# Optimization experiments

Measured on AMD Instinct MI355X. Metric: run time of the kernel, lower is better.

## Reference

```python
import jax, jax.numpy as jnp
import numpy as np

D = 256            # number of graph nodes (example.size(3))
K1 = D // 2        # topkpool1 k
K2 = D // 4        # topkpool2 k
B = 8


def _lrelu(x):
    return jnp.where(x > 0, x, 0.33 * x)


def _e2e(h, wa, ba, wb, bb):
    # h: [B,C,d,d]; wa,wb: [P,C,d] (squeezed (1,d)/(d,1) conv kernels)
    # cnn1: contract over columns j -> [B,P,d]; cnn2: contract over rows i -> [B,P,d]
    a = jnp.einsum('bcij,pcj->bpi', h, wa) + ba[None, :, None]
    b = jnp.einsum('bcij,pci->bpj', h, wb) + bb[None, :, None]
    # cat([a]*d, 3) + cat([b]*d, 2)  ==  broadcast-add
    return a[:, :, :, None] + b[:, :, None, :]


def _gcn(h, g, W, b):
    # h: [B,N,F_in], g: [B,N,N]; faithful to norm_g: g[i,j] / deg[j] (column-normalized
    # because torch broadcasts the [N] degree vector over the LAST dim)
    gb = (g > 0).astype(h.dtype)
    deg = gb.sum(axis=2)                      # [B,N] row sums
    gn = gb / deg[:, None, :]                 # divide column j by deg[j]
    return jnp.einsum('bij,bjf->bif', gn, h) @ W.T + b


def _pool(h, g, s, k):
    # h: [B,N,F], g: [B,N,N], s: [B,N,1] -> top-k nodes by score (descending)
    vals, idx = jax.lax.top_k(s[:, :, 0], k)              # [B,k]
    hn = jnp.take_along_axis(h, idx[:, :, None], axis=1)  # [B,k,F]
    gn = jnp.take_along_axis(g, idx[:, :, None], axis=1)
    gn = jnp.take_along_axis(gn, idx[:, None, :], axis=2) # [B,k,k]
    return hn, gn, vals[:, :, None]


def _readout(h):
    # h: [B,N,F] (node axis = 1); torch ReadOut on [B,F,N,1] max/mean over dim=2
    return jnp.concatenate([h.max(axis=1), h.mean(axis=1)], axis=1)  # [B,2F]


def _forward(x, w1a, b1a, w1b, b1b, w2a, b2a, w2b, b2b, e2n_w, e2n_b,
             a11_w, a11_b, a12_w, a12_b, g1_w, g1_b,
             a21_w, a21_b, a22_w, a22_b,
             d1_w, d1_b, d2_w, d2_b, d3_w, d3_b):
    h = _lrelu(_e2e(x, w1a, b1a, w1b, b1b))         # [B,128,d,d]
    h = _lrelu(_e2e(h, w2a, b2a, w2b, b2b))         # [B,256,d,d]
    # E2N conv (1,d): [B,8,d,1] -> node features [B,d,8]
    nodes = _lrelu(jnp.einsum('bcij,pcj->bpi', h, e2n_w) + e2n_b[None, :, None])
    nodes = jnp.transpose(nodes, (0, 2, 1))          # [B,d,8]
    g0 = x[:, 0]                                     # [B,d,d]

    w = _lrelu(_gcn(nodes, g0, a11_w, a11_b))        # [B,d,1]
    w = jax.nn.sigmoid(_gcn(w, g0, a12_w, a12_b))
    h1, g1, s1 = _pool(nodes, g0, w, K1)             # [B,K1,8], [B,K1,K1], [B,K1,1]
    out = h1 * s1 + h1
    sum1 = _readout(out)                             # [B,16]

    h2 = _gcn(out, g1, g1_w, g1_b)                   # [B,K1,8] (no activation, as in torch)
    w = _lrelu(_gcn(h2, g1, a21_w, a21_b))
    w = jax.nn.sigmoid(_gcn(w, g1, a22_w, a22_b))
    h3, g2, s2 = _pool(h2, g1, w, K2)                # [B,K2,8]
    out2 = h3 * s2 + h3
    sum2 = _readout(out2)                            # [B,16]

    z = sum1 + sum2                                  # [B,16]
    z = _lrelu(z @ d1_w.T + d1_b)                    # dropout = identity (eval mode)
    z = _lrelu(z @ d2_w.T + d2_b)
    return z @ d3_w.T + d3_b                         # [B,1]


def setup_inputs() -> dict:
    key = jax.random.key(0)
    ks = jax.random.split(key, 16)
    f32 = jnp.float32

    def rn(k, shape, scale):
        return jax.random.normal(k, shape, dtype=f32) * scale

    return {
        'x': jax.random.normal(ks[0], (B, 1, D, D), dtype=f32),
        'w1a': rn(ks[1], (128, 1, D), 0.08),  'b1a': jnp.zeros((128,), f32),
        'w1b': rn(ks[2], (128, 1, D), 0.08),  'b1b': jnp.zeros((128,), f32),
        'w2a': rn(ks[3], (256, 128, D), 0.008), 'b2a': jnp.zeros((256,), f32),
        'w2b': rn(ks[4], (256, 128, D), 0.008), 'b2b': jnp.zeros((256,), f32),
        'e2n_w': rn(ks[5], (8, 256, D), 0.005), 'e2n_b': jnp.zeros((8,), f32),
        'a11_w': rn(ks[6], (1, 8), 0.3),  'a11_b': jnp.zeros((1,), f32),
        'a12_w': rn(ks[7], (1, 1), 0.3),  'a12_b': jnp.zeros((1,), f32),
        'g1_w': rn(ks[8], (8, 8), 0.3),   'g1_b': jnp.zeros((8,), f32),
        'a21_w': rn(ks[9], (1, 8), 0.3),  'a21_b': jnp.zeros((1,), f32),
        'a22_w': rn(ks[10], (1, 1), 0.3), 'a22_b': jnp.zeros((1,), f32),
        'd1_w': rn(ks[11], (128, 16), 0.2), 'd1_b': jnp.zeros((128,), f32),
        'd2_w': rn(ks[12], (64, 128), 0.08), 'd2_b': jnp.zeros((64,), f32),
        'd3_w': rn(ks[13], (1, 64), 0.1),  'd3_b': jnp.zeros((1,), f32),
    }


def reference(x, w1a, b1a, w1b, b1b, w2a, b2a, w2b, b2b, e2n_w, e2n_b,
              a11_w, a11_b, a12_w, a12_b, g1_w, g1_b,
              a21_w, a21_b, a22_w, a22_b,
              d1_w, d1_b, d2_w, d2_b, d3_w, d3_b):
    return _forward(x, w1a, b1a, w1b, b1b, w2a, b2a, w2b, b2b, e2n_w, e2n_b,
                    a11_w, a11_b, a12_w, a12_b, g1_w, g1_b,
                    a21_w, a21_b, a22_w, a22_b,
                    d1_w, d1_b, d2_w, d2_b, d3_w, d3_b)
```

## Files before the change

### kernel.cpp

```cpp
#include <hip/hip_runtime.h>

typedef short s16x8 __attribute__((ext_vector_type(8)));
typedef float f32x4 __attribute__((ext_vector_type(4)));
typedef float f32x2 __attribute__((ext_vector_type(2)));

#define TID threadIdx.x

__device__ __forceinline__ float lrelu_f(float x) { return fmaxf(x, 0.33f * x); }

__device__ __forceinline__ unsigned lrelu_pack(float pv, f32x2 q) {
    f32x2 s = q + pv;
    f32x2 m = s * 0.33f;
    f32x2 r = __builtin_elementwise_max(s, m);
    unsigned u;
    asm("v_cvt_pk_bf16_f32 %0, %1, %2" : "=v"(u) : "v"(r.x), "v"(r.y));
    return u;
}
__device__ __forceinline__ unsigned pk_bf16(float a, float b) {
    unsigned u;
    asm("v_cvt_pk_bf16_f32 %0, %1, %2" : "=v"(u) : "v"(a), "v"(b));
    return u;
}

union FragU { s16x8 v; uint4 q; unsigned w[4]; };

__global__ __launch_bounds__(256) void k_convert(
    const float* __restrict__ sa, unsigned short* __restrict__ da, int na4,
    const float* __restrict__ sb, unsigned short* __restrict__ db, int nb4,
    const float* __restrict__ sc, unsigned short* __restrict__ dc, int nc4)
{
    const float* s; unsigned short* d; int n4;
    if (blockIdx.y == 0)      { s = sa; d = da; n4 = na4; }
    else if (blockIdx.y == 1) { s = sb; d = db; n4 = nb4; }
    else                      { s = sc; d = dc; n4 = nc4; }
    const int stride = gridDim.x * 256;
    for (int i = blockIdx.x * 256 + TID; i < n4; i += stride) {
        float4 v = ((const float4*)s)[i];
        ((uint2*)d)[i] = make_uint2(pk_bf16(v.x, v.y), pk_bf16(v.z, v.w));
    }
}

__global__ __launch_bounds__(128) void k_l1(
    const float* __restrict__ x,
    const float* __restrict__ w1a, const float* __restrict__ b1a,
    const float* __restrict__ w1b, const float* __restrict__ b1b,
    float* __restrict__ A1, float* __restrict__ B1)
{
    const int r = blockIdx.x, b = blockIdx.y, v = blockIdx.z;
    const int tid = TID;
    __shared__ float xr[256];
    const float* xb = x + b * 65536;
    if (v == 0) {
        xr[tid]       = xb[r * 256 + tid];
        xr[tid + 128] = xb[r * 256 + tid + 128];
    } else {
        xr[tid]       = xb[tid * 256 + r];
        xr[tid + 128] = xb[(tid + 128) * 256 + r];
    }
    __syncthreads();
    const float* w    = v ? w1b : w1a;
    const float* bias = v ? b1b : b1a;
    float* OUT = v ? B1 : A1;
    float acc = bias[tid];
    const float* wr = w + tid * 256;
    #pragma unroll 4
    for (int q = 0; q < 256; q += 8) {
        float4 a = *(const float4*)(wr + q);
        float4 c = *(const float4*)(wr + q + 4);
        acc += xr[q + 0] * a.x + xr[q + 1] * a.y + xr[q + 2] * a.z + xr[q + 3] * a.w;
        acc += xr[q + 4] * c.x + xr[q + 5] * c.y + xr[q + 6] * c.z + xr[q + 7] * c.w;
    }
    OUT[b * 32768 + tid * 256 + r] = acc;
}

__global__ __launch_bounds__(512) void k_e2e(
    const float* __restrict__ A1, const float* __restrict__ B1,
    const unsigned short* __restrict__ w2aM, const unsigned short* __restrict__ w2bM,
    float* __restrict__ part)
{
    const int bid = blockIdx.x;
    const int xcd = bid & 7, tt = bid >> 3;
    const int hi = tt >> 4, inner = tt & 15;
    const int slice = xcd + 8 * hi;
    const int s = slice >> 1, which = slice & 1;
    const int rt = inner >> 3, b = inner & 7;
    const int bw = b * 2 + which;

    const float* P = (which ? B1 : A1) + b * 32768;
    const float* Q = (which ? A1 : B1) + b * 32768;
    const unsigned short* W = which ? w2bM : w2aM;
    const int c0 = s * 16, r0 = rt * 128;

    __shared__ float Qs[16][256];
    __shared__ float Ps[16][128];
    __shared__ uint4 Hs[2][4096];

    const int tid = TID;
    const int wave = tid >> 6, lane = tid & 63, quad = lane >> 4, l16 = lane & 15;
    const int wi = wave & 3, wj = wave >> 2;
    const int pbase = wi * 64, rbase = wj * 64;
    const int hbase = wj * 4;

    {
        const float4* Qg = (const float4*)(Q + c0 * 256);
        float4* Qd = (float4*)&Qs[0][0];
        Qd[tid]       = Qg[tid];
        Qd[tid + 512] = Qg[tid + 512];
        int row = tid >> 5, col = tid & 31;
        *(float4*)&Ps[row][col * 4] = *(const float4*)&P[(c0 + row) * 256 + r0 + col * 4];
    }
    __syncthreads();

    {
        const int qb = wave * 32 + quad * 8;
        f32x2 q0p = *(const f32x2*)&Qs[0][qb + 0];
        f32x2 q1p = *(const f32x2*)&Qs[0][qb + 2];
        f32x2 q2p = *(const f32x2*)&Qs[0][qb + 4];
        f32x2 q3p = *(const f32x2*)&Qs[0][qb + 6];
        #pragma unroll
        for (int rf = 0; rf < 8; ++rf) {
            float pv = Ps[0][rf * 16 + l16];
            uint4 u;
            u.x = lrelu_pack(pv, q0p);
            u.y = lrelu_pack(pv, q1p);
            u.z = lrelu_pack(pv, q2p);
            u.w = lrelu_pack(pv, q3p);
            Hs[0][(wave * 8 + rf) * 64 + lane] = u;
        }
    }
    __syncthreads();

    f32x4 acc[4][4] = {};

    const unsigned short* Wrow[4];
    #pragma unroll
    for (int pf = 0; pf < 4; ++pf)
        Wrow[pf] = W + (size_t)(pbase + pf * 16 + l16) * 32768 + c0 * 256 + quad * 8;

    FragU af[4][4];
    #pragma unroll
    for (int d = 0; d < 3; ++d)
        #pragma unroll
        for (int pf = 0; pf < 4; ++pf)
            af[d][pf].q = *(const uint4*)(Wrow[pf] + d * 32);

    for (int c = 0; c < 16; ++c) {
        const int cb = c & 1, nb = cb ^ 1;

        f32x2 q0p, q1p, q2p, q3p;
        if (c + 1 < 16) {
            const int qb = wave * 32 + quad * 8;
            q0p = *(const f32x2*)&Qs[c + 1][qb + 0];
            q1p = *(const f32x2*)&Qs[c + 1][qb + 2];
            q2p = *(const f32x2*)&Qs[c + 1][qb + 4];
            q3p = *(const f32x2*)&Qs[c + 1][qb + 6];
        }

        FragU hbf[2][4];
        #pragma unroll
        for (int nf = 0; nf < 4; ++nf)
            hbf[0][nf].q = Hs[cb][(hbase + nf) * 64 + lane];

        #pragma unroll
        for (int q0 = 0; q0 < 8; ++q0) {
            const int cur = q0 & 1, nxt = cur ^ 1;
            const int slot = q0 & 3, nslot = (q0 + 3) & 3;

            {
                const int cn = c + ((q0 + 3) >> 3);
                const int qn = (q0 + 3) & 7;
                if (cn < 16) {
                    #pragma unroll
                    for (int pf = 0; pf < 4; ++pf)
                        af[nslot][pf].q = *(const uint4*)(Wrow[pf] + cn * 256 + qn * 32);
                }
            }
            if (q0 < 7) {
                #pragma unroll
                for (int nf = 0; nf < 4; ++nf)
                    hbf[nxt][nf].q = Hs[cb][((q0 + 1) * 8 + hbase + nf) * 64 + lane];
            }
            if (c + 1 < 16) {
                float pv = Ps[c + 1][q0 * 16 + l16];
                uint4 u;
                u.x = lrelu_pack(pv, q0p);
                u.y = lrelu_pack(pv, q1p);
                u.z = lrelu_pack(pv, q2p);
                u.w = lrelu_pack(pv, q3p);
                Hs[nb][(wave * 8 + q0) * 64 + lane] = u;
            }
            #pragma unroll
            for (int nf = 0; nf < 4; ++nf)
                #pragma unroll
                for (int pf = 0; pf < 4; ++pf)
                    acc[pf][nf] = __builtin_amdgcn_mfma_f32_16x16x32_bf16(af[slot][pf].v, hbf[cur][nf].v, acc[pf][nf], 0, 0, 0);
        }
        __syncthreads();
    }

    float* pb = part + (size_t)(s * 16 + bw) * 65536;
    #pragma unroll
    for (int pf = 0; pf < 4; ++pf)
        #pragma unroll
        for (int nf = 0; nf < 4; ++nf)
            #pragma unroll
            for (int t = 0; t < 4; ++t) {
                int p = pbase + pf * 16 + quad * 4 + t;
                int r = r0 + rbase + nf * 16 + l16;
                pb[p * 256 + r] = acc[pf][nf][t];
            }
}

__global__ __launch_bounds__(256) void k_red(
    const float* __restrict__ part,
    const float* __restrict__ b2a, const float* __restrict__ b2b,
    float* __restrict__ A2, float* __restrict__ B2)
{
    const int bw = blockIdx.y; const int b = bw >> 1, which = bw & 1;
    const int idx = blockIdx.x * 256 + TID;
    const float4* pp = (const float4*)part;
    float4 acc = make_float4(0.f, 0.f, 0.f, 0.f);
    #pragma unroll
    for (int s = 0; s < 8; ++s) {
        float4 v = pp[(size_t)(s * 16 + bw) * 16384 + idx];
        acc.x += v.x; acc.y += v.y; acc.z += v.z; acc.w += v.w;
    }
    const int p = idx >> 6;
    const float bias = (which ? b2b : b2a)[p];
    acc.x += bias; acc.y += bias; acc.z += bias; acc.w += bias;
    float* OUT = (which ? B2 : A2) + b * 65536;
    ((float4*)OUT)[idx] = acc;
}

__global__ __launch_bounds__(256) void k_e2n(
    const float* __restrict__ A2, const float* __restrict__ B2,
    const unsigned short* __restrict__ e2nw,
    float* __restrict__ nodes_raw)
{
    const int it = blockIdx.x, b = blockIdx.y, sn = blockIdx.z;
    const int tid = TID, wave = tid >> 6, lane = tid & 63, quad = lane >> 4, l16 = lane & 15;
    const int i0 = it * 16;
    const int c0 = sn * 32 + wave * 8;
    const float* Ab = A2 + b * 65536;
    const float* Bb = B2 + b * 65536;
    const float* Brow0 = Bb + c0 * 256 + quad * 8;
    const unsigned short* Wrow0 = e2nw + (size_t)l16 * 65536 + c0 * 256 + quad * 8;

    f32x4 acc = {};
    FragU af[2];
    f32x2 qp[2][4];
    float pv, pvn;

    if (l16 < 8) af[0].q = *(const uint4*)(Wrow0);
    else         af[0].q = make_uint4(0u, 0u, 0u, 0u);
    #pragma unroll
    for (int k = 0; k < 4; ++k) qp[0][k] = *(const f32x2*)(Brow0 + 2 * k);
    pv = Ab[c0 * 256 + i0 + l16];

    for (int cc = 0; cc < 8; ++cc) {
        #pragma unroll
        for (int q0 = 0; q0 < 8; ++q0) {
            const int cur = q0 & 1, nxt = cur ^ 1;
            const int cn = (q0 == 7) ? cc + 1 : cc;
            const int qn = (q0 + 1) & 7;
            if (cn < 8) {
                if (l16 < 8) af[nxt].q = *(const uint4*)(Wrow0 + cn * 256 + qn * 32);
                else         af[nxt].q = make_uint4(0u, 0u, 0u, 0u);
                #pragma unroll
                for (int k = 0; k < 4; ++k)
                    qp[nxt][k] = *(const f32x2*)(Brow0 + cn * 256 + qn * 32 + 2 * k);
            }
            if (q0 == 4 && cc + 1 < 8) pvn = Ab[(c0 + cc + 1) * 256 + i0 + l16];
            FragU hb;
            hb.w[0] = lrelu_pack(pv, qp[cur][0]);
            hb.w[1] = lrelu_pack(pv, qp[cur][1]);
            hb.w[2] = lrelu_pack(pv, qp[cur][2]);
            hb.w[3] = lrelu_pack(pv, qp[cur][3]);
            acc = __builtin_amdgcn_mfma_f32_16x16x32_bf16(af[cur].v, hb.v, acc, 0, 0, 0);
            if (q0 == 7) pv = pvn;
        }
    }
    __shared__ float red[4][16][16];
    #pragma unroll
    for (int t = 0; t < 4; ++t) red[wave][quad * 4 + t][l16] = acc[t];
    __syncthreads();
    const int row = tid >> 4, col = tid & 15;
    if (row < 8) {
        float ssum = red[0][row][col] + red[1][row][col] + red[2][row][col] + red[3][row][col];
        atomicAdd(&nodes_raw[b * 2048 + (i0 + col) * 8 + row], ssum);
    }
}

__global__ __launch_bounds__(256) void k_adj(
    const float* __restrict__ x,
    unsigned long long* __restrict__ adjw, float* __restrict__ rdegw)
{
    const int b = blockIdx.y;
    const int tid = TID, wave = tid >> 6, lane = tid & 63;
    const int rbase = blockIdx.x * 32 + wave * 8;
    for (int rr = 0; rr < 8; ++rr) {
        const int row = rbase + rr;
        int d = 0;
        unsigned long long w[4];
        #pragma unroll
        for (int k = 0; k < 4; ++k) {
            float v = x[b * 65536 + row * 256 + k * 64 + lane];
            w[k] = __ballot(v > 0.0f);
            d += __popcll(w[k]);
        }
        if (lane == 0) {
            #pragma unroll
            for (int k = 0; k < 4; ++k) adjw[(b * 256 + row) * 4 + k] = w[k];
            rdegw[b * 256 + row] = d ? 1.0f / (float)d : 0.0f;
        }
    }
}

__global__ __launch_bounds__(256) void k_tail(
    const unsigned long long* __restrict__ adjw, const float* __restrict__ rdegw,
    const float* __restrict__ nodes_raw, const float* __restrict__ e2n_b,
    const float* __restrict__ a11_w, const float* __restrict__ a11_b,
    const float* __restrict__ a12_w, const float* __restrict__ a12_b,
    const float* __restrict__ g1_w,  const float* __restrict__ g1_b,
    const float* __restrict__ a21_w, const float* __restrict__ a21_b,
    const float* __restrict__ a22_w, const float* __restrict__ a22_b,
    const float* __restrict__ d1_w,  const float* __restrict__ d1_b,
    const float* __restrict__ d2_w,  const float* __restrict__ d2_b,
    const float* __restrict__ d3_w,  const float* __restrict__ d3_b,
    float* __restrict__ out)
{
    const int b = blockIdx.x;
    const int tid = TID;

    __shared__ unsigned long long adj[256][4];
    __shared__ float nod[256][8];
    __shared__ float rdeg[256];
    __shared__ float md[256];
    __shared__ float w1s[256];
    __shared__ float w2s[256];
    __shared__ int   selflag[256];
    __shared__ int   selidx[128];
    __shared__ float s1v[128];
    __shared__ float out1[128][8];
    __shared__ float aggL[128][8];
    __shared__ float h2L[128][8];
    __shared__ unsigned long long adj1[128][2];
    __shared__ float rdeg1[128];
    __shared__ float tA[128];
    __shared__ float w1t[128];
    __shared__ float w2t[128];
    __shared__ int   sel2flag[128];
    __shared__ int   sel2idx[64];
    __shared__ float s2v[64];
    __shared__ float out2[64][8];
    __shared__ float r1[16], r2[16], zz[16];
    __shared__ float z1[128];
    __shared__ float z2[64];

    if (tid < 128) { selidx[tid] = 0; s1v[tid] = 0.0f; }
    if (tid < 64)  { sel2idx[tid] = 0; s2v[tid] = 0.0f; }

    {
        #pragma unroll
        for (int k = 0; k < 4; ++k) adj[tid][k] = adjw[(b * 256 + tid) * 4 + k];
        rdeg[tid] = rdegw[b * 256 + tid];
        for (int f = 0; f < 8; ++f)
            nod[tid][f] = lrelu_f(nodes_raw[b * 2048 + tid * 8 + f] + e2n_b[f]);
    }
    __syncthreads();
    {
        float s = 0.0f;
        for (int f = 0; f < 8; ++f) s += nod[tid][f] * a11_w[f];
        md[tid] = s * rdeg[tid];
    }
    __syncthreads();
    {
        float s = 0.0f;
        for (int k = 0; k < 4; ++k) {
            unsigned long long m = adj[tid][k];
            while (m) { int j = __builtin_ctzll(m); m &= m - 1; s += md[k * 64 + j]; }
        }
        w1s[tid] = lrelu_f(s + a11_b[0]);
    }
    __syncthreads();
    md[tid] = w1s[tid] * a12_w[0] * rdeg[tid];
    __syncthreads();
    {
        float s = 0.0f;
        for (int k = 0; k < 4; ++k) {
            unsigned long long m = adj[tid][k];
            while (m) { int j = __builtin_ctzll(m); m &= m - 1; s += md[k * 64 + j]; }
        }
        w2s[tid] = 1.0f / (1.0f + expf(-(s + a12_b[0])));
    }
    __syncthreads();
    {
        const float my = w2s[tid];
        int cnt = 0;
        for (int j = 0; j < 256; ++j) {
            float o = w2s[j];
            cnt += (o > my) || (o == my && j < tid);
        }
        selflag[tid] = (cnt < 128) ? 1 : 0;
    }
    __syncthreads();
    if (selflag[tid]) {
        int pos = 0;
        for (int j = 0; j < tid; ++j) pos += selflag[j];
        if (pos < 128) { selidx[pos] = tid; s1v[pos] = w2s[tid]; }
    }
    __syncthreads();
    for (int k = tid; k < 1024; k += 256) {
        int t = k >> 3, f = k & 7;
        out1[t][f] = nod[selidx[t]][f] * (1.0f + s1v[t]);
    }
    __syncthreads();
    if (tid < 16) {
        int f = tid & 7;
        if (tid < 8) {
            float mx = -INFINITY;
            for (int t = 0; t < 128; ++t) mx = fmaxf(mx, out1[t][f]);
            r1[tid] = mx;
        } else {
            float s = 0.0f;
            for (int t = 0; t < 128; ++t) s += out1[t][f];
            r1[tid] = s * (1.0f / 128.0f);
        }
    }
    if (tid < 128) {
        unsigned long long wds[2] = {0ull, 0ull};
        const int gi = selidx[tid];
        for (int u = 0; u < 128; ++u) {
            const int gj = selidx[u];
            unsigned long long bit = (adj[gi][gj >> 6] >> (gj & 63)) & 1ull;
            wds[u >> 6] |= bit << (u & 63);
        }
        adj1[tid][0] = wds[0]; adj1[tid][1] = wds[1];
        int d = __popcll(wds[0]) + __popcll(wds[1]);
        rdeg1[tid] = d ? 1.0f / (float)d : 0.0f;
    }
    __syncthreads();
    {
        const int t = tid >> 1, f0 = (tid & 1) * 4;
        float a0 = 0, a1 = 0, a2 = 0, a3 = 0;
        for (int k = 0; k < 2; ++k) {
            unsigned long long m = adj1[t][k];
            while (m) {
                int u = __builtin_ctzll(m); m &= m - 1;
                int uu = k * 64 + u;
                float rr = rdeg1[uu];
                a0 += out1[uu][f0 + 0] * rr;
                a1 += out1[uu][f0 + 1] * rr;
                a2 += out1[uu][f0 + 2] * rr;
                a3 += out1[uu][f0 + 3] * rr;
            }
        }
        aggL[t][f0 + 0] = a0; aggL[t][f0 + 1] = a1; aggL[t][f0 + 2] = a2; aggL[t][f0 + 3] = a3;
    }
    __syncthreads();
    for (int k = tid; k < 1024; k += 256) {
        int t = k >> 3, fo = k & 7;
        float s = g1_b[fo];
        for (int f = 0; f < 8; ++f) s += aggL[t][f] * g1_w[fo * 8 + f];
        h2L[t][fo] = s;
    }
    __syncthreads();
    if (tid < 128) {
        float s = 0.0f;
        for (int f = 0; f < 8; ++f) s += h2L[tid][f] * a21_w[f];
        tA[tid] = s * rdeg1[tid];
    }
    __syncthreads();
    if (tid < 128) {
        float s = 0.0f;
        for (int k = 0; k < 2; ++k) {
            unsigned long long m = adj1[tid][k];
            while (m) { int u = __builtin_ctzll(m); m &= m - 1; s += tA[k * 64 + u]; }
        }
        w1t[tid] = lrelu_f(s + a21_b[0]);
    }
    __syncthreads();
    if (tid < 128) tA[tid] = w1t[tid] * a22_w[0] * rdeg1[tid];
    __syncthreads();
    if (tid < 128) {
        float s = 0.0f;
        for (int k = 0; k < 2; ++k) {
            unsigned long long m = adj1[tid][k];
            while (m) { int u = __builtin_ctzll(m); m &= m - 1; s += tA[k * 64 + u]; }
        }
        w2t[tid] = 1.0f / (1.0f + expf(-(s + a22_b[0])));
    }
    __syncthreads();
    if (tid < 128) {
        const float my = w2t[tid];
        int cnt = 0;
        for (int u = 0; u < 128; ++u) {
            float o = w2t[u];
            cnt += (o > my) || (o == my && u < tid);
        }
        sel2flag[tid] = (cnt < 64) ? 1 : 0;
    }
    __syncthreads();
    if (tid < 128 && sel2flag[tid]) {
        int pos = 0;
        for (int u = 0; u < tid; ++u) pos += sel2flag[u];
        if (pos < 64) { sel2idx[pos] = tid; s2v[pos] = w2t[tid]; }
    }
    __syncthreads();
    for (int k = tid; k < 512; k += 256) {
        int u = k >> 3, f = k & 7;
        out2[u][f] = h2L[sel2idx[u]][f] * (1.0f + s2v[u]);
    }
    __syncthreads();
    if (tid < 16) {
        int f = tid & 7;
        if (tid < 8) {
            float mx = -INFINITY;
            for (int t = 0; t < 64; ++t) mx = fmaxf(mx, out2[t][f]);
            r2[tid] = mx;
        } else {
            float s = 0.0f;
            for (int t = 0; t < 64; ++t) s += out2[t][f];
            r2[tid] = s * (1.0f / 64.0f);
        }
    }
    __syncthreads();
    if (tid < 16) zz[tid] = r1[tid] + r2[tid];
    __syncthreads();
    if (tid < 128) {
        float s = d1_b[tid];
        for (int k = 0; k < 16; ++k) s += zz[k] * d1_w[tid * 16 + k];
        z1[tid] = lrelu_f(s);
    }
    __syncthreads();
    if (tid < 64) {
        float s = d2_b[tid];
        for (int k = 0; k < 128; ++k) s += z1[k] * d2_w[tid * 128 + k];
        z2[tid] = lrelu_f(s);
    }
    __syncthreads();
    if (tid == 0) {
        float s = d3_b[0];
        for (int k = 0; k < 64; ++k) s += z2[k] * d3_w[k];
        out[b] = s;
    }
}

extern "C" void kernel_launch(void* const* d_in, const int* in_sizes, int n_in,
                              void* d_out, int out_size, void* d_ws, size_t ws_size,
                              hipStream_t stream) {
    const float* x     = (const float*)d_in[0];
    const float* w1a   = (const float*)d_in[1];
    const float* b1a   = (const float*)d_in[2];
    const float* w1b   = (const float*)d_in[3];
    const float* b1b   = (const float*)d_in[4];
    const float* w2a   = (const float*)d_in[5];
    const float* b2a   = (const float*)d_in[6];
    const float* w2b   = (const float*)d_in[7];
    const float* b2b   = (const float*)d_in[8];
    const float* e2nw  = (const float*)d_in[9];

    float* ws        = (float*)d_ws;
    float* A1        = ws;
    float* B1        = ws + 262144;
    float* A2        = ws + 524288;
    float* B2        = ws + 1048576;
    float* nodes_raw = ws + 1572864;
    float* rdegw     = ws + 1589248;
    unsigned long long* adjw = (unsigned long long*)(ws + 1597440);
    float* part      = ws + 1613824;
    unsigned short* w2aM  = (unsigned short*)(ws + 10002432);
    unsigned short* w2bM  = w2aM + 8388608;
    unsigned short* e2nwM = w2bM + 8388608;

    k_convert<<<dim3(512, 3), 256, 0, stream>>>(
        w2a, w2aM, 8388608 / 4,
        w2b, w2bM, 8388608 / 4,
        e2nw, e2nwM, 524288 / 4);
    hipMemsetAsync(nodes_raw, 0, 16384 * sizeof(float), stream);
    k_l1<<<dim3(256, 8, 2), 128, 0, stream>>>(x, w1a, b1a, w1b, b1b, A1, B1);
    k_adj<<<dim3(8, 8), 256, 0, stream>>>(x, adjw, rdegw);
    k_e2e<<<dim3(256), 512, 0, stream>>>(A1, B1, w2aM, w2bM, part);
    k_red<<<dim3(64, 16), 256, 0, stream>>>(part, b2a, b2b, A2, B2);
    k_e2n<<<dim3(16, 8, 8), 256, 0, stream>>>(A2, B2, e2nwM, nodes_raw);
    k_tail<<<dim3(8), 256, 0, stream>>>(adjw, rdegw, nodes_raw, (const float*)d_in[10],
        (const float*)d_in[11], (const float*)d_in[12], (const float*)d_in[13], (const float*)d_in[14],
        (const float*)d_in[15], (const float*)d_in[16], (const float*)d_in[17], (const float*)d_in[18],
        (const float*)d_in[19], (const float*)d_in[20], (const float*)d_in[21], (const float*)d_in[22],
        (const float*)d_in[23], (const float*)d_in[24], (const float*)d_in[25], (const float*)d_in[26],
        (float*)d_out);
}
```

Before: 438.8 us.

## Shrink e2e row tile to 64 and double grid for higher occupancy

The e2e MFMA kernel now handles 64 rows per block instead of 128, so the grid doubles to 512 blocks. Each wave owns 32 output channels across all 64 rows, which halves the accumulator and weight-fragment registers, and launch bounds now request 4 blocks per CU. The double-buffered H tile is replaced by a single buffer rebuilt between two barriers, and weight prefetch depth drops from three stages to one. This trades latency hiding inside a block and adds a synchronisation per channel for more resident waves and better CU fill, but each Q slice and each weight row is now read by twice as many blocks.

```diff
diff --git a/kernel.cpp b/kernel.cpp
--- a/kernel.cpp
+++ b/kernel.cpp
@@ -73,14 +73,14 @@
     OUT[b * 32768 + tid * 256 + r] = acc;
 }
 
-__global__ __launch_bounds__(512) void k_e2e(
+__global__ __launch_bounds__(512, 4) void k_e2e(
     const float* __restrict__ A1, const float* __restrict__ B1,
     const unsigned short* __restrict__ w2aM, const unsigned short* __restrict__ w2bM,
     float* __restrict__ part)
 {
     const int bid = blockIdx.x;
     const int xcd = bid & 7, tt = bid >> 3;
-    const int hi = tt >> 4, inner = tt & 15;
+    const int hi = tt >> 5, inner = tt & 31;
     const int slice = xcd + 8 * hi;
     const int s = slice >> 1, which = slice & 1;
     const int rt = inner >> 3, b = inner & 7;
@@ -89,124 +89,112 @@
     const float* P = (which ? B1 : A1) + b * 32768;
     const float* Q = (which ? A1 : B1) + b * 32768;
     const unsigned short* W = which ? w2bM : w2aM;
-    const int c0 = s * 16, r0 = rt * 128;
+    const int c0 = s * 16, r0 = rt * 64;
 
     __shared__ float Qs[16][256];
-    __shared__ float Ps[16][128];
-    __shared__ uint4 Hs[2][4096];
+    __shared__ float Ps[16][64];
+    __shared__ uint4 Hs[2048];
 
     const int tid = TID;
     const int wave = tid >> 6, lane = tid & 63, quad = lane >> 4, l16 = lane & 15;
-    const int wi = wave & 3, wj = wave >> 2;
-    const int pbase = wi * 64, rbase = wj * 64;
-    const int hbase = wj * 4;
+    const int pbase = wave * 32;
 
     {
         const float4* Qg = (const float4*)(Q + c0 * 256);
         float4* Qd = (float4*)&Qs[0][0];
         Qd[tid]       = Qg[tid];
         Qd[tid + 512] = Qg[tid + 512];
-        int row = tid >> 5, col = tid & 31;
-        *(float4*)&Ps[row][col * 4] = *(const float4*)&P[(c0 + row) * 256 + r0 + col * 4];
+        int row = tid >> 5, c2 = (tid & 31) * 2;
+        *(float2*)&Ps[row][c2] = *(const float2*)&P[(c0 + row) * 256 + r0 + c2];
     }
     __syncthreads();
 
     {
         const int qb = wave * 32 + quad * 8;
-        f32x2 q0p = *(const f32x2*)&Qs[0][qb + 0];
-        f32x2 q1p = *(const f32x2*)&Qs[0][qb + 2];
-        f32x2 q2p = *(const f32x2*)&Qs[0][qb + 4];
-        f32x2 q3p = *(const f32x2*)&Qs[0][qb + 6];
-        #pragma unroll
-        for (int rf = 0; rf < 8; ++rf) {
+        f32x2 qp0 = *(const f32x2*)&Qs[0][qb + 0];
+        f32x2 qp1 = *(const f32x2*)&Qs[0][qb + 2];
+        f32x2 qp2 = *(const f32x2*)&Qs[0][qb + 4];
+        f32x2 qp3 = *(const f32x2*)&Qs[0][qb + 6];
+        #pragma unroll
+        for (int rf = 0; rf < 4; ++rf) {
             float pv = Ps[0][rf * 16 + l16];
             uint4 u;
-            u.x = lrelu_pack(pv, q0p);
-            u.y = lrelu_pack(pv, q1p);
-            u.z = lrelu_pack(pv, q2p);
-            u.w = lrelu_pack(pv, q3p);
-            Hs[0][(wave * 8 + rf) * 64 + lane] = u;
-        }
-    }
-    __syncthreads();
-
-    f32x4 acc[4][4] = {};
-
-    const unsigned short* Wrow[4];
+            u.x = lrelu_pack(pv, qp0);
+            u.y = lrelu_pack(pv, qp1);
+            u.z = lrelu_pack(pv, qp2);
+            u.w = lrelu_pack(pv, qp3);
+            Hs[(wave * 4 + rf) * 64 + lane] = u;
+        }
+    }
+
+    f32x4 acc[2][4] = {};
+    const unsigned short* Wrow[2];
     #pragma unroll
-    for (int pf = 0; pf < 4; ++pf)
+    for (int pf = 0; pf < 2; ++pf)
         Wrow[pf] = W + (size_t)(pbase + pf * 16 + l16) * 32768 + c0 * 256 + quad * 8;
 
-    FragU af[4][4];
+    FragU af[2][2];
     #pragma unroll
-    for (int d = 0; d < 3; ++d)
-        #pragma unroll
-        for (int pf = 0; pf < 4; ++pf)
-            af[d][pf].q = *(const uint4*)(Wrow[pf] + d * 32);
+    for (int pf = 0; pf < 2; ++pf) af[0][pf].q = *(const uint4*)(Wrow[pf]);
+
+    __syncthreads();
 
     for (int c = 0; c < 16; ++c) {
-        const int cb = c & 1, nb = cb ^ 1;
-
-        f32x2 q0p, q1p, q2p, q3p;
-        if (c + 1 < 16) {
-            const int qb = wave * 32 + quad * 8;
-            q0p = *(const f32x2*)&Qs[c + 1][qb + 0];
-            q1p = *(const f32x2*)&Qs[c + 1][qb + 2];
-            q2p = *(const f32x2*)&Qs[c + 1][qb + 4];
-            q3p = *(const f32x2*)&Qs[c + 1][qb + 6];
-        }
-
         FragU hbf[2][4];
         #pragma unroll
         for (int nf = 0; nf < 4; ++nf)
-            hbf[0][nf].q = Hs[cb][(hbase + nf) * 64 + lane];
+            hbf[0][nf].q = Hs[nf * 64 + lane];
 
         #pragma unroll
         for (int q0 = 0; q0 < 8; ++q0) {
             const int cur = q0 & 1, nxt = cur ^ 1;
-            const int slot = q0 & 3, nslot = (q0 + 3) & 3;
-
-            {
-                const int cn = c + ((q0 + 3) >> 3);
-                const int qn = (q0 + 3) & 7;
-                if (cn < 16) {
-                    #pragma unroll
-                    for (int pf = 0; pf < 4; ++pf)
-                        af[nslot][pf].q = *(const uint4*)(Wrow[pf] + cn * 256 + qn * 32);
-                }
+            const int cn = c + ((q0 + 1) >> 3), qn = (q0 + 1) & 7;
+            if (cn < 16) {
+                #pragma unroll
+                for (int pf = 0; pf < 2; ++pf)
+                    af[nxt][pf].q = *(const uint4*)(Wrow[pf] + cn * 256 + qn * 32);
             }
             if (q0 < 7) {
                 #pragma unroll
                 for (int nf = 0; nf < 4; ++nf)
-                    hbf[nxt][nf].q = Hs[cb][((q0 + 1) * 8 + hbase + nf) * 64 + lane];
-            }
-            if (c + 1 < 16) {
-                float pv = Ps[c + 1][q0 * 16 + l16];
-                uint4 u;
-                u.x = lrelu_pack(pv, q0p);
-                u.y = lrelu_pack(pv, q1p);
-                u.z = lrelu_pack(pv, q2p);
-                u.w = lrelu_pack(pv, q3p);
-                Hs[nb][(wave * 8 + q0) * 64 + lane] = u;
+                    hbf[nxt][nf].q = Hs[((q0 + 1) * 4 + nf) * 64 + lane];
             }
             #pragma unroll
             for (int nf = 0; nf < 4; ++nf)
                 #pragma unroll
-                for (int pf = 0; pf < 4; ++pf)
-                    acc[pf][nf] = __builtin_amdgcn_mfma_f32_16x16x32_bf16(af[slot][pf].v, hbf[cur][nf].v, acc[pf][nf], 0, 0, 0);
+                for (int pf = 0; pf < 2; ++pf)
+                    acc[pf][nf] = __builtin_amdgcn_mfma_f32_16x16x32_bf16(af[cur][pf].v, hbf[cur][nf].v, acc[pf][nf], 0, 0, 0);
         }
         __syncthreads();
+        if (c + 1 < 16) {
+            const int qb = wave * 32 + quad * 8;
+            f32x2 qp0 = *(const f32x2*)&Qs[c + 1][qb + 0];
+            f32x2 qp1 = *(const f32x2*)&Qs[c + 1][qb + 2];
+            f32x2 qp2 = *(const f32x2*)&Qs[c + 1][qb + 4];
+            f32x2 qp3 = *(const f32x2*)&Qs[c + 1][qb + 6];
+            #pragma unroll
+            for (int rf = 0; rf < 4; ++rf) {
+                float pv = Ps[c + 1][rf * 16 + l16];
+                uint4 u;
+                u.x = lrelu_pack(pv, qp0);
+                u.y = lrelu_pack(pv, qp1);
+                u.z = lrelu_pack(pv, qp2);
+                u.w = lrelu_pack(pv, qp3);
+                Hs[(wave * 4 + rf) * 64 + lane] = u;
+            }
+            __syncthreads();
+        }
     }
 
     float* pb = part + (size_t)(s * 16 + bw) * 65536;
     #pragma unroll
-    for (int pf = 0; pf < 4; ++pf)
+    for (int pf = 0; pf < 2; ++pf)
         #pragma unroll
         for (int nf = 0; nf < 4; ++nf)
             #pragma unroll
             for (int t = 0; t < 4; ++t) {
                 int p = pbase + pf * 16 + quad * 4 + t;
-                int r = r0 + rbase + nf * 16 + l16;
+                int r = r0 + nf * 16 + l16;
                 pb[p * 256 + r] = acc[pf][nf][t];
             }
 }
@@ -580,7 +568,7 @@
     hipMemsetAsync(nodes_raw, 0, 16384 * sizeof(float), stream);
     k_l1<<<dim3(256, 8, 2), 128, 0, stream>>>(x, w1a, b1a, w1b, b1b, A1, B1);
     k_adj<<<dim3(8, 8), 256, 0, stream>>>(x, adjw, rdegw);
-    k_e2e<<<dim3(256), 512, 0, stream>>>(A1, B1, w2aM, w2bM, part);
+    k_e2e<<<dim3(512), 512, 0, stream>>>(A1, B1, w2aM, w2bM, part);
     k_red<<<dim3(64, 16), 256, 0, stream>>>(part, b2a, b2b, A2, B2);
     k_e2n<<<dim3(16, 8, 8), 256, 0, stream>>>(A2, B2, e2nwM, nodes_raw);
     k_tail<<<dim3(8), 256, 0, stream>>>(adjw, rdegw, nodes_raw, (const float*)d_in[10],
```

Result: no change. 441.2 us (+0.5%).
